# Optimization experiments

Measured on AMD Instinct MI355X. Metric: run time of the kernel, lower is better.

Reference implementation:

```python
import jax, jax.numpy as jnp
import numpy as np
import math

DIM = 768
K1 = 112
K2 = 224


def setup_inputs() -> dict:
    key = jax.random.key(0)
    ks = jax.random.split(key, 10)
    B, N, D = 256, 196, DIM
    inp = {
        "rgb_patches": jax.random.normal(ks[0], (B, N, D), jnp.float32),
        "nir_patches": jax.random.normal(ks[1], (B, N, D), jnp.float32),
        "tir_patches": jax.random.normal(ks[2], (B, N, D), jnp.float32),
        "rgb_global": jax.random.normal(ks[3], (B, D), jnp.float32),
        "nir_global": jax.random.normal(ks[4], (B, D), jnp.float32),
        "tir_global": jax.random.normal(ks[5], (B, D), jnp.float32),
        # nn.Linear params (W_v is defined in the torch module but never used in forward)
        "Wq": jax.random.normal(ks[6], (D, D), jnp.float32) / math.sqrt(D),
        "bq": jnp.zeros((D,), jnp.float32),
        "Wk": jax.random.normal(ks[7], (D, D), jnp.float32) / math.sqrt(D),
        "bk": jnp.zeros((D,), jnp.float32),
    }
    return inp


def _scatter_ones(idx, B, n):
    # idx: [B, K] in [0, n] where value n means "drop" (scattered into pad slot)
    rows = jnp.arange(B)[:, None]
    m = jnp.zeros((B, n + 1), jnp.float32).at[rows, idx].set(1.0)
    return m[:, :n]


def _intra_mask(patches, g, scale):
    # scores over own-modality patches
    B, N, _ = patches.shape
    scores = jax.nn.softmax(jnp.einsum('bd,bnd->bn', g, patches) * scale, axis=1)
    _, idx = jax.lax.top_k(scores, min(K1, N))
    return _scatter_ones(idx, B, N)


def _split_scatter(idx, B, n_a, n_b):
    # idx indexes concat([a (len n_a), b (len n_b)]); route to two masks
    idx_a = jnp.where(idx < n_a, idx, n_a)          # pad slot n_a when not a
    idx_b = jnp.where(idx >= n_a, idx - n_a, n_b)   # pad slot n_b when not b
    return _scatter_ones(idx_a, B, n_a), _scatter_ones(idx_b, B, n_b)


def reference(rgb_patches, nir_patches, tir_patches, rgb_global, nir_global, tir_global, Wq, bq, Wk, bk):
    B, n_rgb, D = rgb_patches.shape
    n_nir = nir_patches.shape[1]
    n_tir = tir_patches.shape[1]
    scale = 1.0 / math.sqrt(D)

    # ---- intra-modal selection ----
    rgb_mask_i = _intra_mask(rgb_patches, rgb_global, scale)
    nir_mask_i = _intra_mask(nir_patches, nir_global, scale)
    tir_mask_i = _intra_mask(tir_patches, tir_global, scale)

    # ---- inter-modal selection ----
    queries = jnp.stack([rgb_global, nir_global, tir_global], axis=1)        # [B,3,D]
    keys = jnp.concatenate([rgb_patches, nir_patches, tir_patches], axis=1)  # [B,3N,D]
    q = queries @ Wq.T + bq
    k = keys @ Wk.T + bk
    scores = jax.nn.softmax(jnp.einsum('bqd,bnd->bqn', q, k) * scale, axis=2)

    rgb_scores = jnp.concatenate([scores[:, 0, n_rgb:n_rgb + n_nir], scores[:, 0, n_rgb + n_nir:]], axis=1)
    nir_scores = jnp.concatenate([scores[:, 1, :n_rgb], scores[:, 1, n_rgb + n_nir:]], axis=1)
    tir_scores = jnp.concatenate([scores[:, 2, :n_rgb], scores[:, 2, n_rgb:n_rgb + n_nir]], axis=1)

    _, rgb_idx = jax.lax.top_k(rgb_scores, min(K2, rgb_scores.shape[1]))
    _, nir_idx = jax.lax.top_k(nir_scores, min(K2, nir_scores.shape[1]))
    _, tir_idx = jax.lax.top_k(tir_scores, min(K2, tir_scores.shape[1]))

    # rgb query selects among [nir, tir]; nir query among [rgb, tir]; tir query among [rgb, nir]
    nir_m1, tir_m1 = _split_scatter(rgb_idx, B, n_nir, n_tir)
    rgb_m1, tir_m2 = _split_scatter(nir_idx, B, n_rgb, n_tir)
    rgb_m2, nir_m2 = _split_scatter(tir_idx, B, n_rgb, n_nir)

    rgb_mask_c = jnp.maximum(rgb_m1, rgb_m2)
    nir_mask_c = jnp.maximum(nir_m1, nir_m2)
    tir_mask_c = jnp.maximum(tir_m1, tir_m2)

    # ---- union of masks, apply ----
    rgb_mask = (rgb_mask_c + rgb_mask_i > 0).astype(rgb_patches.dtype)[..., None]
    nir_mask = (nir_mask_c + nir_mask_i > 0).astype(nir_patches.dtype)[..., None]
    tir_mask = (tir_mask_c + tir_mask_i > 0).astype(tir_patches.dtype)[..., None]

    return (rgb_patches * rgb_mask, nir_patches * nir_mask, tir_patches * tir_mask)
```

## Files before the change

kernel.cpp:

```cpp
#include <hip/hip_runtime.h>

#define DD   768
#define BB   256
#define NN   196
#define KK1  112
#define KK2  224
#define RTOT (BB*3)
#define CAND (2*NN)

typedef float vfloat4 __attribute__((ext_vector_type(4)));


__global__ __launch_bounds__(256) void gemm_q(
    const float* __restrict__ g0, const float* __restrict__ g1,
    const float* __restrict__ g2, const float* __restrict__ Wq,
    const float* __restrict__ bq, double* __restrict__ Qh)
{
    __shared__ float As[32][33];
    __shared__ float Ws[32][33];
    const int t  = threadIdx.x;
    const int tx = t & 15, ty = t >> 4;
    const int i0 = blockIdx.y * 32, j0 = blockIdx.x * 32;
    double a00 = 0, a01 = 0, a10 = 0, a11 = 0;
    for (int kk = 0; kk < DD; kk += 32) {
        for (int s = 0; s < 4; ++s) {
            int idx = t + s * 256;
            int r = idx >> 5, c = idx & 31;
            int row = i0 + r;
            int b = row / 3, q = row - b * 3;
            const float* gp = (q == 0) ? g0 : (q == 1) ? g1 : g2;
            As[r][c] = gp[b * DD + kk + c];
            Ws[r][c] = Wq[(j0 + r) * DD + kk + c];
        }
        __syncthreads();
        for (int k = 0; k < 32; ++k) {
            double x0 = (double)As[ty][k],      x1 = (double)As[ty + 16][k];
            double y0 = (double)Ws[tx][k],      y1 = (double)Ws[tx + 16][k];
            a00 += x0 * y0; a01 += x0 * y1; a10 += x1 * y0; a11 += x1 * y1;
        }
        __syncthreads();
    }
    Qh[(i0 + ty) * DD + j0 + tx]           = a00 + (double)bq[j0 + tx];
    Qh[(i0 + ty) * DD + j0 + tx + 16]      = a01 + (double)bq[j0 + tx + 16];
    Qh[(i0 + ty + 16) * DD + j0 + tx]      = a10 + (double)bq[j0 + tx];
    Qh[(i0 + ty + 16) * DD + j0 + tx + 16] = a11 + (double)bq[j0 + tx + 16];
}

__global__ __launch_bounds__(256) void gemm_t(
    const double* __restrict__ Qh, const float* __restrict__ Wk,
    double* __restrict__ Td)
{
    __shared__ double As[32][33];
    __shared__ float  Ws[32][33];
    const int t  = threadIdx.x;
    const int tx = t & 15, ty = t >> 4;
    const int i0 = blockIdx.y * 32, j0 = blockIdx.x * 32;
    double a00 = 0, a01 = 0, a10 = 0, a11 = 0;
    for (int kk = 0; kk < DD; kk += 32) {
        for (int s = 0; s < 4; ++s) {
            int idx = t + s * 256;
            int r = idx >> 5, c = idx & 31;
            As[r][c] = Qh[(i0 + r) * DD + kk + c];
            Ws[r][c] = Wk[(kk + r) * DD + j0 + c];
        }
        __syncthreads();
        for (int k = 0; k < 32; ++k) {
            double x0 = As[ty][k],            x1 = As[ty + 16][k];
            double y0 = (double)Ws[k][tx],    y1 = (double)Ws[k][tx + 16];
            a00 += x0 * y0; a01 += x0 * y1; a10 += x1 * y0; a11 += x1 * y1;
        }
        __syncthreads();
    }
    Td[(i0 + ty) * DD + j0 + tx]           = a00;
    Td[(i0 + ty) * DD + j0 + tx + 16]      = a01;
    Td[(i0 + ty + 16) * DD + j0 + tx]      = a10;
    Td[(i0 + ty + 16) * DD + j0 + tx + 16] = a11;
}

__global__ __launch_bounds__(1024) void fused_score_rank_apply(
    const float* __restrict__ p0, const float* __restrict__ p1,
    const float* __restrict__ p2, const float* __restrict__ g0,
    const float* __restrict__ g1, const float* __restrict__ g2,
    const double* __restrict__ Td, float* __restrict__ out)
{
    const int b = blockIdx.x;
    __shared__ float  Gf[3][DD];
    __shared__ double Tq[3][DD];
    __shared__ double Li[3][NN];
    __shared__ double Le[3][CAND];
    __shared__ unsigned char msk[3][NN];

    for (int d = threadIdx.x; d < DD; d += 1024) {
        Gf[0][d] = g0[b * DD + d];
        Gf[1][d] = g1[b * DD + d];
        Gf[2][d] = g2[b * DD + d];
        Tq[0][d] = Td[(b * 3 + 0) * DD + d];
        Tq[1][d] = Td[(b * 3 + 1) * DD + d];
        Tq[2][d] = Td[(b * 3 + 2) * DD + d];
    }
    if (threadIdx.x < 3 * NN) (&msk[0][0])[threadIdx.x] = 0;
    __syncthreads();

    const int wave = threadIdx.x >> 6, lane = threadIdx.x & 63;

    for (int r = wave; r < 3 * NN; r += 16) {
        const int m = r / NN, n = r - m * NN;
        const float* pp = (m == 0) ? p0 : (m == 1) ? p1 : p2;
        const vfloat4* row = (const vfloat4*)(pp + (size_t)(b * NN + n) * DD);
        vfloat4* orow = (vfloat4*)(out + ((size_t)m * (BB * NN) + b * NN + n) * (size_t)DD);
        const int qa = (m == 0) ? 1 : 0;
        const int qb = (m == 2) ? 1 : 2;
        const int slota = m - (m > qa ? 1 : 0);
        const int slotb = m - (m > qb ? 1 : 0);
        double s0 = 0, s1 = 0, s2 = 0;
        for (int c = lane; c < DD / 4; c += 64) {
            vfloat4 v = row[c];
            __builtin_nontemporal_store(v, &orow[c]);
            const int d = c * 4;
            s0 += (double)Gf[m][d]     * (double)v[0] + (double)Gf[m][d + 1] * (double)v[1]
                + (double)Gf[m][d + 2] * (double)v[2] + (double)Gf[m][d + 3] * (double)v[3];
            s1 += Tq[qa][d]     * (double)v[0] + Tq[qa][d + 1] * (double)v[1]
                + Tq[qa][d + 2] * (double)v[2] + Tq[qa][d + 3] * (double)v[3];
            s2 += Tq[qb][d]     * (double)v[0] + Tq[qb][d + 1] * (double)v[1]
                + Tq[qb][d + 2] * (double)v[2] + Tq[qb][d + 3] * (double)v[3];
        }
        for (int off = 32; off > 0; off >>= 1) {
            s0 += __shfl_down(s0, off);
            s1 += __shfl_down(s1, off);
            s2 += __shfl_down(s2, off);
        }
        if (lane == 0) {
            Li[m][n] = s0;
            Le[qa][slota * NN + n] = s1;
            Le[qb][slotb * NN + n] = s2;
        }
    }
    __syncthreads();

    if (threadIdx.x < 3 * NN) {
        const int m = threadIdx.x / NN, n = threadIdx.x - m * NN;
        const double v = Li[m][n];
        int rank = 0;
        for (int j = 0; j < NN; ++j) {
            double u = Li[m][j];
            rank += (u > v) || (u == v && j < n);
        }
        if (rank < KK1) msk[m][n] = 1;
    }
    for (int t = threadIdx.x; t < 3 * CAND; t += 1024) {
        const int q = t / CAND, c = t - q * CAND;
        const double v = Le[q][c];
        int rank = 0;
        for (int j = 0; j < CAND; ++j) {
            double u = Le[q][j];
            rank += (u > v) || (u == v && j < c);
        }
        if (rank < KK2) {
            const int ma = (q == 0) ? 1 : 0;
            const int mb = (q == 2) ? 1 : 2;
            const int mm  = (c < NN) ? ma : mb;
            const int tok = (c < NN) ? c : c - NN;
            msk[mm][tok] = 1;
        }
    }
    __syncthreads();

    for (int r = wave; r < 3 * NN; r += 16) {
        const int m = r / NN, n = r - m * NN;
        if (!msk[m][n]) {
            vfloat4* orow = (vfloat4*)(out + ((size_t)m * (BB * NN) + b * NN + n) * (size_t)DD);
            const vfloat4 z = {0.f, 0.f, 0.f, 0.f};
            for (int c = lane; c < DD / 4; c += 64)
                __builtin_nontemporal_store(z, &orow[c]);
        }
    }
}

extern "C" void kernel_launch(void* const* d_in, const int* in_sizes, int n_in,
                              void* d_out, int out_size, void* d_ws, size_t ws_size,
                              hipStream_t stream) {
    const float* p0 = (const float*)d_in[0];
    const float* p1 = (const float*)d_in[1];
    const float* p2 = (const float*)d_in[2];
    const float* g0 = (const float*)d_in[3];
    const float* g1 = (const float*)d_in[4];
    const float* g2 = (const float*)d_in[5];
    const float* Wq = (const float*)d_in[6];
    const float* bq = (const float*)d_in[7];
    const float* Wk = (const float*)d_in[8];

    char* ws = (char*)d_ws;
    double* Qh = (double*)(ws);
    double* Td = (double*)(ws + 4718592);

    dim3 ggrid(DD / 32, RTOT / 32);
    gemm_q<<<ggrid, 256, 0, stream>>>(g0, g1, g2, Wq, bq, Qh);
    gemm_t<<<ggrid, 256, 0, stream>>>(Qh, Wk, Td);
    fused_score_rank_apply<<<BB, 1024, 0, stream>>>(p0, p1, p2, g0, g1, g2, Td, (float*)d_out);
}
```

Measured before the change: 921.8 us.

## Split-K the two FP64 projection GEMMs into four chunks with separate reduction

```diff
diff --git a/kernel.cpp b/kernel.cpp
--- a/kernel.cpp
+++ b/kernel.cpp
@@ -7,22 +7,26 @@
 #define KK2  224
 #define RTOT (BB*3)
 #define CAND (2*NN)
+#define NSK  4
+#define KCH  (DD/NSK)
+#define MAT  (DD*DD)
 
 typedef float vfloat4 __attribute__((ext_vector_type(4)));
 
 
-__global__ __launch_bounds__(256) void gemm_q(
+__global__ __launch_bounds__(256) void gemm_q_sk(
     const float* __restrict__ g0, const float* __restrict__ g1,
     const float* __restrict__ g2, const float* __restrict__ Wq,
-    const float* __restrict__ bq, double* __restrict__ Qh)
+    double* __restrict__ Qh4)
 {
     __shared__ float As[32][33];
     __shared__ float Ws[32][33];
     const int t  = threadIdx.x;
     const int tx = t & 15, ty = t >> 4;
     const int i0 = blockIdx.y * 32, j0 = blockIdx.x * 32;
+    const int kc = blockIdx.z;
     double a00 = 0, a01 = 0, a10 = 0, a11 = 0;
-    for (int kk = 0; kk < DD; kk += 32) {
+    for (int kk = kc * KCH; kk < kc * KCH + KCH; kk += 32) {
         for (int s = 0; s < 4; ++s) {
             int idx = t + s * 256;
             int r = idx >> 5, c = idx & 31;
@@ -40,23 +44,35 @@
         }
         __syncthreads();
     }
-    Qh[(i0 + ty) * DD + j0 + tx]           = a00 + (double)bq[j0 + tx];
-    Qh[(i0 + ty) * DD + j0 + tx + 16]      = a01 + (double)bq[j0 + tx + 16];
-    Qh[(i0 + ty + 16) * DD + j0 + tx]      = a10 + (double)bq[j0 + tx];
-    Qh[(i0 + ty + 16) * DD + j0 + tx + 16] = a11 + (double)bq[j0 + tx + 16];
-}
-
-__global__ __launch_bounds__(256) void gemm_t(
+    double* Q = Qh4 + (size_t)kc * MAT;
+    Q[(i0 + ty) * DD + j0 + tx]           = a00;
+    Q[(i0 + ty) * DD + j0 + tx + 16]      = a01;
+    Q[(i0 + ty + 16) * DD + j0 + tx]      = a10;
+    Q[(i0 + ty + 16) * DD + j0 + tx + 16] = a11;
+}
+
+__global__ __launch_bounds__(256) void reduce_q(
+    const double* __restrict__ Qh4, const float* __restrict__ bq,
+    double* __restrict__ Qh)
+{
+    const int i = blockIdx.x * 256 + threadIdx.x;
+    const int e = i - (i / DD) * DD;
+    double s = ((Qh4[i] + Qh4[i + MAT]) + Qh4[i + 2 * MAT]) + Qh4[i + 3 * MAT];
+    Qh[i] = s + (double)bq[e];
+}
+
+__global__ __launch_bounds__(256) void gemm_t_sk(
     const double* __restrict__ Qh, const float* __restrict__ Wk,
-    double* __restrict__ Td)
+    double* __restrict__ Td4)
 {
     __shared__ double As[32][33];
     __shared__ float  Ws[32][33];
     const int t  = threadIdx.x;
     const int tx = t & 15, ty = t >> 4;
     const int i0 = blockIdx.y * 32, j0 = blockIdx.x * 32;
+    const int kc = blockIdx.z;
     double a00 = 0, a01 = 0, a10 = 0, a11 = 0;
-    for (int kk = 0; kk < DD; kk += 32) {
+    for (int kk = kc * KCH; kk < kc * KCH + KCH; kk += 32) {
         for (int s = 0; s < 4; ++s) {
             int idx = t + s * 256;
             int r = idx >> 5, c = idx & 31;
@@ -71,17 +87,18 @@
         }
         __syncthreads();
     }
-    Td[(i0 + ty) * DD + j0 + tx]           = a00;
-    Td[(i0 + ty) * DD + j0 + tx + 16]      = a01;
-    Td[(i0 + ty + 16) * DD + j0 + tx]      = a10;
-    Td[(i0 + ty + 16) * DD + j0 + tx + 16] = a11;
+    double* T = Td4 + (size_t)kc * MAT;
+    T[(i0 + ty) * DD + j0 + tx]           = a00;
+    T[(i0 + ty) * DD + j0 + tx + 16]      = a01;
+    T[(i0 + ty + 16) * DD + j0 + tx]      = a10;
+    T[(i0 + ty + 16) * DD + j0 + tx + 16] = a11;
 }
 
 __global__ __launch_bounds__(1024) void fused_score_rank_apply(
     const float* __restrict__ p0, const float* __restrict__ p1,
     const float* __restrict__ p2, const float* __restrict__ g0,
     const float* __restrict__ g1, const float* __restrict__ g2,
-    const double* __restrict__ Td, float* __restrict__ out)
+    const double* __restrict__ Td4, float* __restrict__ out)
 {
     const int b = blockIdx.x;
     __shared__ float  Gf[3][DD];
@@ -94,9 +111,12 @@
         Gf[0][d] = g0[b * DD + d];
         Gf[1][d] = g1[b * DD + d];
         Gf[2][d] = g2[b * DD + d];
-        Tq[0][d] = Td[(b * 3 + 0) * DD + d];
-        Tq[1][d] = Td[(b * 3 + 1) * DD + d];
-        Tq[2][d] = Td[(b * 3 + 2) * DD + d];
+        #pragma unroll
+        for (int q = 0; q < 3; ++q) {
+            const size_t off = (size_t)(b * 3 + q) * DD + d;
+            Tq[q][d] = ((Td4[off] + Td4[off + MAT]) + Td4[off + 2 * MAT])
+                     + Td4[off + 3 * MAT];
+        }
     }
     if (threadIdx.x < 3 * NN) (&msk[0][0])[threadIdx.x] = 0;
     __syncthreads();
@@ -190,11 +210,13 @@
     const float* Wk = (const float*)d_in[8];
 
     char* ws = (char*)d_ws;
-    double* Qh = (double*)(ws);
-    double* Td = (double*)(ws + 4718592);
-
-    dim3 ggrid(DD / 32, RTOT / 32);
-    gemm_q<<<ggrid, 256, 0, stream>>>(g0, g1, g2, Wq, bq, Qh);
-    gemm_t<<<ggrid, 256, 0, stream>>>(Qh, Wk, Td);
-    fused_score_rank_apply<<<BB, 1024, 0, stream>>>(p0, p1, p2, g0, g1, g2, Td, (float*)d_out);
-}
+    double* Qh4 = (double*)(ws);
+    double* Qh  = (double*)(ws + 18874368);
+    double* Td4 = (double*)(ws + 23592960);
+
+    dim3 ggrid(DD / 32, RTOT / 32, NSK);
+    gemm_q_sk<<<ggrid, 256, 0, stream>>>(g0, g1, g2, Wq, Qh4);
+    reduce_q<<<MAT / 256, 256, 0, stream>>>(Qh4, bq, Qh);
+    gemm_t_sk<<<ggrid, 256, 0, stream>>>(Qh, Wk, Td4);
+    fused_score_rank_apply<<<BB, 1024, 0, stream>>>(p0, p1, p2, g0, g1, g2, Td4, (float*)d_out);
+}
```

After: 895.8 us. -2.8%, faster.
